# Optimization experiments

Hardware: AMD Instinct MI355X
Metric: run time of the kernel (lower is better)

## Reference

```python
import jax, jax.numpy as jnp
import numpy as np

D_NODE, D_PAIR, H = 512, 128, 16
HD = D_NODE // H  # head_dim = 32
B, N = 2, 1024


def _layernorm(x, gamma, beta, eps=1e-5):
    mu = jnp.mean(x, axis=-1, keepdims=True)
    var = jnp.var(x, axis=-1, keepdims=True)
    return (x - mu) * jax.lax.rsqrt(var + eps) * gamma + beta


def setup_inputs() -> dict:
    key = jax.random.key(0)
    ks = jax.random.split(key, 16)
    sc = 0.02
    inp = {
        's': jax.random.normal(ks[0], (B, N, D_NODE), jnp.float32),
        'z': jax.random.normal(ks[1], (B, N, N, D_PAIR), jnp.float32),
        'key_mask': jax.random.randint(ks[2], (B, N), 0, 2).astype(bool),
        'Wq': jax.random.normal(ks[3], (D_NODE, D_NODE), jnp.float32) * sc,
        'bq': jnp.zeros((D_NODE,), jnp.float32),
        'Wk': jax.random.normal(ks[4], (D_NODE, D_NODE), jnp.float32) * sc,
        'bk': jnp.zeros((D_NODE,), jnp.float32),
        'Wv': jax.random.normal(ks[5], (D_NODE, D_NODE), jnp.float32) * sc,
        'bv': jnp.zeros((D_NODE,), jnp.float32),
        'Wb': jax.random.normal(ks[6], (D_PAIR, H), jnp.float32) * sc,
        'bb': jnp.zeros((H,), jnp.float32),
        'Wg': jax.random.normal(ks[7], (D_NODE, D_NODE), jnp.float32) * sc,
        'bg': jnp.zeros((D_NODE,), jnp.float32),
        'Wo': jax.random.normal(ks[8], (D_NODE, D_NODE), jnp.float32) * sc,
        'bo': jnp.zeros((D_NODE,), jnp.float32),
        'gamma': jnp.ones((D_NODE,), jnp.float32),
        'beta': jnp.zeros((D_NODE,), jnp.float32),
    }
    return inp


def reference(s, z, key_mask, Wq, bq, Wk, bk, Wv, bv, Wb, bb, Wg, bg, Wo, bo, gamma, beta):
    b, n, _ = s.shape
    sn = _layernorm(s, gamma, beta)
    q = (sn @ Wq + bq).reshape(b, n, H, HD)
    k = (sn @ Wk + bk).reshape(b, n, H, HD)
    v = (sn @ Wv + bv).reshape(b, n, H, HD)
    # scores: [B, N(query), N(key), H]
    scores = jnp.einsum('bnhd,bmhd->bnmh', q, k) / np.sqrt(HD).astype(np.float32)
    scores = scores + (z @ Wb + bb)  # additive pair bias
    # mask keys (dim 2); True = masked out
    scores = jnp.where(key_mask[:, None, :, None], -jnp.inf, scores)
    attn = jax.nn.softmax(scores, axis=2)
    attn = jnp.nan_to_num(attn, nan=0.0)
    out = jnp.einsum('bnmh,bmhd->bnhd', attn, v).reshape(b, n, D_NODE)
    gate = jax.nn.sigmoid(sn @ Wg + bg)
    return gate * (out @ Wo + bo)
```

## Files before the change

### kernel.cpp

```cpp
#include <hip/hip_runtime.h>
#include <hip/hip_fp16.h>

typedef __attribute__((ext_vector_type(8))) _Float16 f16x8;
typedef __attribute__((ext_vector_type(8))) unsigned short u16x8;
typedef __attribute__((ext_vector_type(4))) float f32x4;

#define DEV __device__ __forceinline__

DEV unsigned short f2h(float f) {
  _Float16 h = (_Float16)f;
  return __builtin_bit_cast(unsigned short, h);
}
DEV float h2f(unsigned short u) {
  return (float)__builtin_bit_cast(_Float16, u);
}
DEV unsigned pk(float lo, float hi) {
  return (unsigned)f2h(lo) | ((unsigned)f2h(hi) << 16);
}

__global__ __launch_bounds__(256) void k_mask(const unsigned* __restrict__ raw,
                                              int* __restrict__ canon) {
  __shared__ int s_gt1, s_f32;
  int t = threadIdx.x;
  if (t == 0) { s_gt1 = 0; s_f32 = 0; }
  __syncthreads();
  int gt1 = 0, fv = 0;
  for (int i = t; i < 512; i += 256) {
    unsigned v = raw[i];
    if (v == 0x3F800000u) fv = 1;
    else if (v > 1u) gt1 = 1;
  }
  if (gt1) s_gt1 = 1;
  if (fv)  s_f32 = 1;
  __syncthreads();
  int mode = s_gt1 ? 1 : (s_f32 ? 2 : 0);
  for (int i = t; i < 2048; i += 256) {
    int v;
    if (mode == 1)      v = ((const unsigned char*)raw)[i] ? 1 : 0;
    else if (mode == 2) v = (((const float*)raw)[i] != 0.f) ? 1 : 0;
    else                v = raw[i] ? 1 : 0;
    canon[i] = v;
  }
}

__global__ __launch_bounds__(64) void k_ln(const float* __restrict__ s,
                                           const float* __restrict__ gamma,
                                           const float* __restrict__ beta,
                                           unsigned short* __restrict__ sn) {
  int row = blockIdx.x, l = threadIdx.x;
  const float* sr = s + (size_t)row * 512 + l * 8;
  float4 x0 = *(const float4*)sr, x1 = *(const float4*)(sr + 4);
  float sum = x0.x + x0.y + x0.z + x0.w + x1.x + x1.y + x1.z + x1.w;
  float sq  = x0.x*x0.x + x0.y*x0.y + x0.z*x0.z + x0.w*x0.w
            + x1.x*x1.x + x1.y*x1.y + x1.z*x1.z + x1.w*x1.w;
#pragma unroll
  for (int off = 32; off >= 1; off >>= 1) {
    sum += __shfl_xor(sum, off);
    sq  += __shfl_xor(sq, off);
  }
  float mu = sum * (1.f / 512.f);
  float rstd = rsqrtf(sq * (1.f / 512.f) - mu * mu + 1e-5f);
  float4 g0 = *(const float4*)(gamma + l * 8), g1 = *(const float4*)(gamma + l * 8 + 4);
  float4 b0 = *(const float4*)(beta + l * 8),  b1 = *(const float4*)(beta + l * 8 + 4);
  u16x8 o;
  o[0] = f2h((x0.x - mu) * rstd * g0.x + b0.x);
  o[1] = f2h((x0.y - mu) * rstd * g0.y + b0.y);
  o[2] = f2h((x0.z - mu) * rstd * g0.z + b0.z);
  o[3] = f2h((x0.w - mu) * rstd * g0.w + b0.w);
  o[4] = f2h((x1.x - mu) * rstd * g1.x + b1.x);
  o[5] = f2h((x1.y - mu) * rstd * g1.y + b1.y);
  o[6] = f2h((x1.z - mu) * rstd * g1.z + b1.z);
  o[7] = f2h((x1.w - mu) * rstd * g1.w + b1.w);
  *(u16x8*)(sn + (size_t)row * 512 + l * 8) = o;
}

DEV void gemm_body(const unsigned short* __restrict__ A,
                   const float* __restrict__ W,
                   const float* __restrict__ bvec,
                   void* __restrict__ outp,
                   const float* __restrict__ gate,
                   int mode, int ct, int rt) {
  int t = threadIdx.x, l = t & 63, w = t >> 6;
  __shared__ unsigned short As[128 * 40];
  __shared__ unsigned short Bs[128 * 40];
  f32x4 acc[4][4];
#pragma unroll
  for (int mt = 0; mt < 4; ++mt)
#pragma unroll
    for (int nt = 0; nt < 4; ++nt) acc[mt][nt] = (f32x4){0.f, 0.f, 0.f, 0.f};

  int arow = t >> 1, akc = (t & 1) * 16;
  int bkk = t >> 3, bc0 = (t & 7) * 16;
  int wr = w >> 1, wc = w & 1;

  for (int k0 = 0; k0 < 512; k0 += 32) {
    const u16x8* ap = (const u16x8*)(A + (size_t)(rt * 128 + arow) * 512 + k0 + akc);
    u16x8 a0 = ap[0], a1 = ap[1];
    *(u16x8*)(&As[arow * 40 + akc]) = a0;
    *(u16x8*)(&As[arow * 40 + akc + 8]) = a1;
    const float* wp = W + (size_t)(k0 + bkk) * 512 + ct * 128 + bc0;
#pragma unroll
    for (int i = 0; i < 4; ++i) {
      float4 f = *(const float4*)(wp + i * 4);
      Bs[(bc0 + i * 4 + 0) * 40 + bkk] = f2h(f.x);
      Bs[(bc0 + i * 4 + 1) * 40 + bkk] = f2h(f.y);
      Bs[(bc0 + i * 4 + 2) * 40 + bkk] = f2h(f.z);
      Bs[(bc0 + i * 4 + 3) * 40 + bkk] = f2h(f.w);
    }
    __syncthreads();
    f16x8 af[4], bf[4];
#pragma unroll
    for (int mt = 0; mt < 4; ++mt)
      af[mt] = *(const f16x8*)(&As[(wr * 64 + mt * 16 + (l & 15)) * 40 + (l >> 4) * 8]);
#pragma unroll
    for (int nt = 0; nt < 4; ++nt)
      bf[nt] = *(const f16x8*)(&Bs[(wc * 64 + nt * 16 + (l & 15)) * 40 + (l >> 4) * 8]);
#pragma unroll
    for (int mt = 0; mt < 4; ++mt)
#pragma unroll
      for (int nt = 0; nt < 4; ++nt)
        acc[mt][nt] = __builtin_amdgcn_mfma_f32_16x16x32_f16(af[mt], bf[nt], acc[mt][nt], 0, 0, 0);
    __syncthreads();
  }

#pragma unroll
  for (int mt = 0; mt < 4; ++mt)
#pragma unroll
    for (int nt = 0; nt < 4; ++nt) {
      int col = ct * 128 + wc * 64 + nt * 16 + (l & 15);
      float bv = bvec[col];
#pragma unroll
      for (int i = 0; i < 4; ++i) {
        int row = rt * 128 + wr * 64 + mt * 16 + (l >> 4) * 4 + i;
        float val = acc[mt][nt][i] + bv;
        int bb_ = row >> 10, n = row & 1023, hh = col >> 5, d = col & 31;
        if (mode == 0) {
          ((unsigned short*)outp)[(size_t)row * 512 + col] = f2h(val);
        } else if (mode == 1) {
          ((unsigned short*)outp)[(((size_t)bb_ * 16 + hh) * 1024 + n) * 32 + d] = f2h(val);
        } else if (mode == 2) {
          ((unsigned short*)outp)[(((size_t)bb_ * 16 + hh) * 32 + d) * 1024 + n] = f2h(val);
        } else if (mode == 3) {
          ((float*)outp)[(size_t)row * 512 + col] = 1.f / (1.f + __expf(-val));
        } else {
          ((float*)outp)[(size_t)row * 512 + col] = gate[(size_t)row * 512 + col] * val;
        }
      }
    }
}

__global__ __launch_bounds__(256) void k_qkvg(const unsigned short* __restrict__ A,
                                              const float* __restrict__ W0, const float* __restrict__ W1,
                                              const float* __restrict__ W2, const float* __restrict__ W3,
                                              const float* __restrict__ b0, const float* __restrict__ b1,
                                              const float* __restrict__ b2, const float* __restrict__ b3,
                                              void* o0, void* o1, void* o2, void* o3) {
  int mode = blockIdx.z;
  const float* W = (mode == 0) ? W0 : (mode == 1) ? W1 : (mode == 2) ? W2 : W3;
  const float* bv = (mode == 0) ? b0 : (mode == 1) ? b1 : (mode == 2) ? b2 : b3;
  void* o = (mode == 0) ? o0 : (mode == 1) ? o1 : (mode == 2) ? o2 : o3;
  gemm_body(A, W, bv, o, nullptr, mode, blockIdx.x, blockIdx.y);
}

__global__ __launch_bounds__(256) void k_gemm_out(const unsigned short* __restrict__ A,
                                                  const float* __restrict__ W,
                                                  const float* __restrict__ bvec,
                                                  float* __restrict__ outp,
                                                  const float* __restrict__ gate) {
  gemm_body(A, W, bvec, outp, gate, 4, blockIdx.x, blockIdx.y);
}

__global__ __launch_bounds__(512) void k_bias(const float* __restrict__ z,
                                              const float* __restrict__ Wb,
                                              const float* __restrict__ bbp,
                                              const int* __restrict__ maskc,
                                              unsigned short* __restrict__ bias) {
  int bid = blockIdx.x;
  int b = bid >> 10;
  int t = threadIdx.x, l = t & 63, w = t >> 6;
  int lane15 = l & 15, g = l >> 4;

  f16x8 wf[4];
#pragma unroll
  for (int ks = 0; ks < 4; ++ks)
#pragma unroll
    for (int j = 0; j < 8; ++j)
      wf[ks][j] = (_Float16)Wb[(ks * 32 + g * 8 + j) * 16 + lane15];
  float bbh = bbp[lane15];

  const float* zb = z + (size_t)bid * (1024 * 128);
  unsigned short* ob = bias + ((size_t)bid * 16 + lane15) * 1024;
  const int* mrow = maskc + b * 1024;

#pragma unroll 2
  for (int mt = 0; mt < 8; ++mt) {
    int m0 = w * 128 + mt * 16;
    const float* zr = zb + (size_t)(m0 + lane15) * 128 + g * 8;
    f32x4 acc = (f32x4){0.f, 0.f, 0.f, 0.f};
#pragma unroll
    for (int ks = 0; ks < 4; ++ks) {
      float4 z0 = *(const float4*)(zr + ks * 32);
      float4 z1 = *(const float4*)(zr + ks * 32 + 4);
      f16x8 af;
      af[0] = (_Float16)z0.x; af[1] = (_Float16)z0.y;
      af[2] = (_Float16)z0.z; af[3] = (_Float16)z0.w;
      af[4] = (_Float16)z1.x; af[5] = (_Float16)z1.y;
      af[6] = (_Float16)z1.z; af[7] = (_Float16)z1.w;
      acc = __builtin_amdgcn_mfma_f32_16x16x32_f16(af, wf[ks], acc, 0, 0, 0);
    }
    int m = m0 + 4 * g;
    int4 mk = *(const int4*)(mrow + m);
    ushort4 o4;
    o4.x = mk.x ? 0xFBFFu : f2h(acc[0] + bbh);
    o4.y = mk.y ? 0xFBFFu : f2h(acc[1] + bbh);
    o4.z = mk.z ? 0xFBFFu : f2h(acc[2] + bbh);
    o4.w = mk.w ? 0xFBFFu : f2h(acc[3] + bbh);
    *(ushort4*)(ob + m) = o4;
  }
}

__global__ __launch_bounds__(256, 4) void k_attn(const unsigned short* __restrict__ qbuf,
                                                 const unsigned short* __restrict__ kbuf,
                                                 const unsigned short* __restrict__ vbuf,
                                                 const unsigned short* __restrict__ bias,
                                                 unsigned short* __restrict__ aout) {
  int qt = blockIdx.x, h = blockIdx.y, b = blockIdx.z;
  int t = threadIdx.x, l = t & 63, w = t >> 6;
  int q0 = (qt * 4 + w) * 16;
  int lane15 = l & 15, g = l >> 4;
  int bh = b * 16 + h;
  const float RS = 0.17677669529663687f;

  f16x8 qf = *(const f16x8*)(qbuf + ((size_t)(b * 1024 + q0 + lane15)) * 512 + h * 32 + g * 8);

  const unsigned short* kb_ = kbuf + (size_t)bh * 1024 * 32;
  const unsigned short* vb_ = vbuf + (size_t)bh * 32 * 1024;
  const unsigned short* brow = bias + ((size_t)(b * 1024 + q0 + lane15) * 16 + h) * 1024;

  float m_run = -3.0e38f, lsum = 0.f;
  f32x4 acc1 = (f32x4){0.f, 0.f, 0.f, 0.f};
  f32x4 acc2 = (f32x4){0.f, 0.f, 0.f, 0.f};

  for (int c = 0; c < 32; ++c) {
    int m0 = c * 32;
    f16x8 kf1 = *(const f16x8*)(kb_ + (size_t)(m0 + lane15) * 32 + g * 8);
    f16x8 kf2 = *(const f16x8*)(kb_ + (size_t)(m0 + 16 + lane15) * 32 + g * 8);
    f32x4 zero = (f32x4){0.f, 0.f, 0.f, 0.f};
    f32x4 c1 = __builtin_amdgcn_mfma_f32_16x16x32_f16(kf1, qf, zero, 0, 0, 0);
    f32x4 c2 = __builtin_amdgcn_mfma_f32_16x16x32_f16(kf2, qf, zero, 0, 0, 0);
    ushort4 bv1 = *(const ushort4*)(brow + m0 + 4 * g);
    ushort4 bv2 = *(const ushort4*)(brow + m0 + 16 + 4 * g);
    float s1[4], s2[4];
    s1[0] = c1[0] * RS + h2f(bv1.x); s1[1] = c1[1] * RS + h2f(bv1.y);
    s1[2] = c1[2] * RS + h2f(bv1.z); s1[3] = c1[3] * RS + h2f(bv1.w);
    s2[0] = c2[0] * RS + h2f(bv2.x); s2[1] = c2[1] * RS + h2f(bv2.y);
    s2[2] = c2[2] * RS + h2f(bv2.z); s2[3] = c2[3] * RS + h2f(bv2.w);
    float cm = fmaxf(fmaxf(fmaxf(s1[0], s1[1]), fmaxf(s1[2], s1[3])),
                     fmaxf(fmaxf(s2[0], s2[1]), fmaxf(s2[2], s2[3])));
    cm = fmaxf(cm, __shfl_xor(cm, 16));
    cm = fmaxf(cm, __shfl_xor(cm, 32));
    float mn = fmaxf(m_run, cm);
    float corr = __expf(m_run - mn);
    m_run = mn;
    float p1[4], p2[4], csum = 0.f;
#pragma unroll
    for (int i = 0; i < 4; ++i) { p1[i] = __expf(s1[i] - mn); csum += p1[i]; }
#pragma unroll
    for (int i = 0; i < 4; ++i) { p2[i] = __expf(s2[i] - mn); csum += p2[i]; }
    lsum = lsum * corr + csum;
#pragma unroll
    for (int i = 0; i < 4; ++i) { acc1[i] *= corr; acc2[i] *= corr; }
    unsigned a0 = pk(p1[0], p1[1]), a1 = pk(p1[2], p1[3]);
    unsigned b0 = pk(p2[0], p2[1]), b1 = pk(p2[2], p2[3]);
    int s0 = ((g & 1) << 5) + lane15, s1l = s0 + 16;
    unsigned wA0 = (unsigned)__shfl((int)a0, s0);
    unsigned wA1 = (unsigned)__shfl((int)a1, s0);
    unsigned wA2 = (unsigned)__shfl((int)a0, s1l);
    unsigned wA3 = (unsigned)__shfl((int)a1, s1l);
    unsigned wB0 = (unsigned)__shfl((int)b0, s0);
    unsigned wB1 = (unsigned)__shfl((int)b1, s0);
    unsigned wB2 = (unsigned)__shfl((int)b0, s1l);
    unsigned wB3 = (unsigned)__shfl((int)b1, s1l);
    bool hi = (l & 32) != 0;
    union { unsigned u[4]; f16x8 v; } pu;
    pu.u[0] = hi ? wB0 : wA0;
    pu.u[1] = hi ? wB1 : wA1;
    pu.u[2] = hi ? wB2 : wA2;
    pu.u[3] = hi ? wB3 : wA3;
    f16x8 vf1 = *(const f16x8*)(vb_ + (size_t)lane15 * 1024 + m0 + 8 * g);
    f16x8 vf2 = *(const f16x8*)(vb_ + (size_t)(16 + lane15) * 1024 + m0 + 8 * g);
    acc1 = __builtin_amdgcn_mfma_f32_16x16x32_f16(vf1, pu.v, acc1, 0, 0, 0);
    acc2 = __builtin_amdgcn_mfma_f32_16x16x32_f16(vf2, pu.v, acc2, 0, 0, 0);
  }

  lsum += __shfl_xor(lsum, 16);
  lsum += __shfl_xor(lsum, 32);
  float inv = (m_run > -30000.f && lsum > 0.f) ? 1.f / lsum : 0.f;
  unsigned short* orow = aout + ((size_t)(b * 1024 + q0 + lane15)) * 512 + h * 32;
  ushort4 o1, o2;
  o1.x = f2h(acc1[0] * inv); o1.y = f2h(acc1[1] * inv);
  o1.z = f2h(acc1[2] * inv); o1.w = f2h(acc1[3] * inv);
  o2.x = f2h(acc2[0] * inv); o2.y = f2h(acc2[1] * inv);
  o2.z = f2h(acc2[2] * inv); o2.w = f2h(acc2[3] * inv);
  *(ushort4*)(orow + 4 * g) = o1;
  *(ushort4*)(orow + 16 + 4 * g) = o2;
}

extern "C" void kernel_launch(void* const* d_in, const int* in_sizes, int n_in,
                              void* d_out, int out_size, void* d_ws, size_t ws_size,
                              hipStream_t stream) {
  (void)in_sizes; (void)n_in; (void)out_size; (void)ws_size;
  const float* s     = (const float*)d_in[0];
  const float* z     = (const float*)d_in[1];
  const unsigned* km = (const unsigned*)d_in[2];
  const float* Wq = (const float*)d_in[3];
  const float* bq = (const float*)d_in[4];
  const float* Wk = (const float*)d_in[5];
  const float* bk = (const float*)d_in[6];
  const float* Wv = (const float*)d_in[7];
  const float* bv = (const float*)d_in[8];
  const float* Wb = (const float*)d_in[9];
  const float* bb = (const float*)d_in[10];
  const float* Wg = (const float*)d_in[11];
  const float* bg = (const float*)d_in[12];
  const float* Wo = (const float*)d_in[13];
  const float* bo = (const float*)d_in[14];
  const float* gamma = (const float*)d_in[15];
  const float* beta  = (const float*)d_in[16];

  char* ws = (char*)d_ws;
  unsigned short* sn    = (unsigned short*)(ws);
  unsigned short* qbuf  = (unsigned short*)(ws + (2ull << 20));
  unsigned short* kbuf  = (unsigned short*)(ws + (4ull << 20));
  unsigned short* vbuf  = (unsigned short*)(ws + (6ull << 20));
  float*          gate  = (float*)(ws + (8ull << 20));
  unsigned short* aout  = (unsigned short*)(ws + (12ull << 20));
  unsigned short* bias  = (unsigned short*)(ws + (14ull << 20));
  int*            maskc = (int*)(ws + (78ull << 20));

  hipLaunchKernelGGL(k_mask, dim3(1), dim3(256), 0, stream, km, maskc);
  hipLaunchKernelGGL(k_ln, dim3(2048), dim3(64), 0, stream, s, gamma, beta, sn);
  hipLaunchKernelGGL(k_qkvg, dim3(4, 16, 4), dim3(256), 0, stream, sn,
                     Wq, Wk, Wv, Wg, bq, bk, bv, bg,
                     (void*)qbuf, (void*)kbuf, (void*)vbuf, (void*)gate);
  hipLaunchKernelGGL(k_bias, dim3(2048), dim3(512), 0, stream, z, Wb, bb, maskc, bias);
  hipLaunchKernelGGL(k_attn, dim3(16, 16, 2), dim3(256), 0, stream,
                     qbuf, kbuf, vbuf, bias, aout);
  hipLaunchKernelGGL(k_gemm_out, dim3(4, 16), dim3(256), 0, stream, aout, Wo, bo,
                     (float*)d_out, gate);
}
```

Measured before the change: 352.6 us.

## Stage z tiles through swizzled LDS in bias kernel; split attention keys across waves

The pair-bias kernel now loads z in fully coalesced contiguous rows into a per-wave swizzled LDS buffer, register-prefetching the next tile while it computes on the current one. This replaces strided per-lane global reads of z, and z is the dominant memory stream. The attention kernel doubles its block to 512 threads, so two waves split the key range for each query tile and merge partial softmax states through LDS. This doubles parallelism at the cost of an extra reduction and a barrier.

```diff
diff --git a/kernel.cpp b/kernel.cpp
--- a/kernel.cpp
+++ b/kernel.cpp
@@ -170,15 +170,19 @@
   gemm_body(A, W, bvec, outp, gate, 4, blockIdx.x, blockIdx.y);
 }
 
-__global__ __launch_bounds__(512) void k_bias(const float* __restrict__ z,
-                                              const float* __restrict__ Wb,
-                                              const float* __restrict__ bbp,
-                                              const int* __restrict__ maskc,
-                                              unsigned short* __restrict__ bias) {
+__global__ __launch_bounds__(256, 4) void k_bias(const float* __restrict__ z,
+                                                 const float* __restrict__ Wb,
+                                                 const float* __restrict__ bbp,
+                                                 const int* __restrict__ maskc,
+                                                 unsigned short* __restrict__ bias) {
   int bid = blockIdx.x;
-  int b = bid >> 10;
+  int slab = bid >> 1, half = bid & 1;
+  int b = slab >> 10;
   int t = threadIdx.x, l = t & 63, w = t >> 6;
   int lane15 = l & 15, g = l >> 4;
+
+  __shared__ float lds_[4][2048];
+  float* wlds = lds_[w];
 
   f16x8 wf[4];
 #pragma unroll
@@ -188,19 +192,35 @@
       wf[ks][j] = (_Float16)Wb[(ks * 32 + g * 8 + j) * 16 + lane15];
   float bbh = bbp[lane15];
 
-  const float* zb = z + (size_t)bid * (1024 * 128);
-  unsigned short* ob = bias + ((size_t)bid * 16 + lane15) * 1024;
+  const char* zb = (const char*)(z + ((size_t)slab * 1024 + half * 512 + (size_t)w * 128) * 128);
+  unsigned short* ob = bias + ((size_t)slab * 16 + lane15) * 1024;
   const int* mrow = maskc + b * 1024;
 
-#pragma unroll 2
-  for (int mt = 0; mt < 8; ++mt) {
-    int m0 = w * 128 + mt * 16;
-    const float* zr = zb + (size_t)(m0 + lane15) * 128 + g * 8;
+  float4 rbuf[8];
+#pragma unroll
+  for (int i = 0; i < 8; ++i)
+    rbuf[i] = *(const float4*)(zb + i * 1024 + l * 16);
+#pragma unroll
+  for (int i = 0; i < 8; ++i) {
+    int lin = i * 1024 + l * 16;
+    int off = lin ^ (((lin >> 9) & 7) << 4);
+    *(float4*)((char*)wlds + off) = rbuf[i];
+  }
+
+  for (int t8 = 0; t8 < 8; ++t8) {
+    if (t8 < 7) {
+      const char* tb = zb + (t8 + 1) * 8192;
+#pragma unroll
+      for (int i = 0; i < 8; ++i)
+        rbuf[i] = *(const float4*)(tb + i * 1024 + l * 16);
+    }
     f32x4 acc = (f32x4){0.f, 0.f, 0.f, 0.f};
 #pragma unroll
     for (int ks = 0; ks < 4; ++ks) {
-      float4 z0 = *(const float4*)(zr + ks * 32);
-      float4 z1 = *(const float4*)(zr + ks * 32 + 4);
+      int linA = lane15 * 512 + ks * 128 + g * 32;
+      int swz = ((lane15 & 7) << 4);
+      float4 z0 = *(const float4*)((const char*)wlds + (linA ^ swz));
+      float4 z1 = *(const float4*)((const char*)wlds + ((linA + 16) ^ swz));
       f16x8 af;
       af[0] = (_Float16)z0.x; af[1] = (_Float16)z0.y;
       af[2] = (_Float16)z0.z; af[3] = (_Float16)z0.w;
@@ -208,40 +228,54 @@
       af[6] = (_Float16)z1.z; af[7] = (_Float16)z1.w;
       acc = __builtin_amdgcn_mfma_f32_16x16x32_f16(af, wf[ks], acc, 0, 0, 0);
     }
-    int m = m0 + 4 * g;
-    int4 mk = *(const int4*)(mrow + m);
+    int mabs = half * 512 + w * 128 + t8 * 16 + 4 * g;
+    int4 mk = *(const int4*)(mrow + mabs);
     ushort4 o4;
     o4.x = mk.x ? 0xFBFFu : f2h(acc[0] + bbh);
     o4.y = mk.y ? 0xFBFFu : f2h(acc[1] + bbh);
     o4.z = mk.z ? 0xFBFFu : f2h(acc[2] + bbh);
     o4.w = mk.w ? 0xFBFFu : f2h(acc[3] + bbh);
-    *(ushort4*)(ob + m) = o4;
-  }
-}
-
-__global__ __launch_bounds__(256, 4) void k_attn(const unsigned short* __restrict__ qbuf,
+    *(ushort4*)(ob + mabs) = o4;
+    if (t8 < 7) {
+#pragma unroll
+      for (int i = 0; i < 8; ++i) {
+        int lin = i * 1024 + l * 16;
+        int off = lin ^ (((lin >> 9) & 7) << 4);
+        *(float4*)((char*)wlds + off) = rbuf[i];
+      }
+    }
+  }
+}
+
+__global__ __launch_bounds__(512, 4) void k_attn(const unsigned short* __restrict__ qbuf,
                                                  const unsigned short* __restrict__ kbuf,
                                                  const unsigned short* __restrict__ vbuf,
                                                  const unsigned short* __restrict__ bias,
                                                  unsigned short* __restrict__ aout) {
   int qt = blockIdx.x, h = blockIdx.y, b = blockIdx.z;
   int t = threadIdx.x, l = t & 63, w = t >> 6;
-  int q0 = (qt * 4 + w) * 16;
+  int qs = w & 3, half = w >> 2;
+  int q0 = (qt * 4 + qs) * 16;
   int lane15 = l & 15, g = l >> 4;
   int bh = b * 16 + h;
   const float RS = 0.17677669529663687f;
 
+  __shared__ float red_m[4][64];
+  __shared__ float red_l[4][64];
+  __shared__ f32x4 red_a1[4][64];
+  __shared__ f32x4 red_a2[4][64];
+
   f16x8 qf = *(const f16x8*)(qbuf + ((size_t)(b * 1024 + q0 + lane15)) * 512 + h * 32 + g * 8);
 
-  const unsigned short* kb_ = kbuf + (size_t)bh * 1024 * 32;
-  const unsigned short* vb_ = vbuf + (size_t)bh * 32 * 1024;
-  const unsigned short* brow = bias + ((size_t)(b * 1024 + q0 + lane15) * 16 + h) * 1024;
+  const unsigned short* kb_ = kbuf + (size_t)bh * 1024 * 32 + (size_t)half * 512 * 32;
+  const unsigned short* vb_ = vbuf + (size_t)bh * 32 * 1024 + half * 512;
+  const unsigned short* brow = bias + ((size_t)(b * 1024 + q0 + lane15) * 16 + h) * 1024 + half * 512;
 
   float m_run = -3.0e38f, lsum = 0.f;
   f32x4 acc1 = (f32x4){0.f, 0.f, 0.f, 0.f};
   f32x4 acc2 = (f32x4){0.f, 0.f, 0.f, 0.f};
 
-  for (int c = 0; c < 32; ++c) {
+  for (int c = 0; c < 16; ++c) {
     int m0 = c * 32;
     f16x8 kf1 = *(const f16x8*)(kb_ + (size_t)(m0 + lane15) * 32 + g * 8);
     f16x8 kf2 = *(const f16x8*)(kb_ + (size_t)(m0 + 16 + lane15) * 32 + g * 8);
@@ -295,15 +329,34 @@
 
   lsum += __shfl_xor(lsum, 16);
   lsum += __shfl_xor(lsum, 32);
-  float inv = (m_run > -30000.f && lsum > 0.f) ? 1.f / lsum : 0.f;
-  unsigned short* orow = aout + ((size_t)(b * 1024 + q0 + lane15)) * 512 + h * 32;
-  ushort4 o1, o2;
-  o1.x = f2h(acc1[0] * inv); o1.y = f2h(acc1[1] * inv);
-  o1.z = f2h(acc1[2] * inv); o1.w = f2h(acc1[3] * inv);
-  o2.x = f2h(acc2[0] * inv); o2.y = f2h(acc2[1] * inv);
-  o2.z = f2h(acc2[2] * inv); o2.w = f2h(acc2[3] * inv);
-  *(ushort4*)(orow + 4 * g) = o1;
-  *(ushort4*)(orow + 16 + 4 * g) = o2;
+
+  if (half) {
+    red_m[qs][l] = m_run;
+    red_l[qs][l] = lsum;
+    red_a1[qs][l] = acc1;
+    red_a2[qs][l] = acc2;
+  }
+  __syncthreads();
+  if (!half) {
+    float pm = red_m[qs][l], plv = red_l[qs][l];
+    f32x4 pa1 = red_a1[qs][l], pa2 = red_a2[qs][l];
+    float mm = fmaxf(m_run, pm);
+    float c1s = __expf(m_run - mm), c2s = __expf(pm - mm);
+    float lt = lsum * c1s + plv * c2s;
+    float inv = (mm > -30000.f && lt > 0.f) ? 1.f / lt : 0.f;
+    unsigned short* orow = aout + ((size_t)(b * 1024 + q0 + lane15)) * 512 + h * 32;
+    ushort4 o1, o2;
+    o1.x = f2h((acc1[0] * c1s + pa1[0] * c2s) * inv);
+    o1.y = f2h((acc1[1] * c1s + pa1[1] * c2s) * inv);
+    o1.z = f2h((acc1[2] * c1s + pa1[2] * c2s) * inv);
+    o1.w = f2h((acc1[3] * c1s + pa1[3] * c2s) * inv);
+    o2.x = f2h((acc2[0] * c1s + pa2[0] * c2s) * inv);
+    o2.y = f2h((acc2[1] * c1s + pa2[1] * c2s) * inv);
+    o2.z = f2h((acc2[2] * c1s + pa2[2] * c2s) * inv);
+    o2.w = f2h((acc2[3] * c1s + pa2[3] * c2s) * inv);
+    *(ushort4*)(orow + 4 * g) = o1;
+    *(ushort4*)(orow + 16 + 4 * g) = o2;
+  }
 }
 
 extern "C" void kernel_launch(void* const* d_in, const int* in_sizes, int n_in,
@@ -343,8 +396,8 @@
   hipLaunchKernelGGL(k_qkvg, dim3(4, 16, 4), dim3(256), 0, stream, sn,
                      Wq, Wk, Wv, Wg, bq, bk, bv, bg,
                      (void*)qbuf, (void*)kbuf, (void*)vbuf, (void*)gate);
-  hipLaunchKernelGGL(k_bias, dim3(2048), dim3(512), 0, stream, z, Wb, bb, maskc, bias);
-  hipLaunchKernelGGL(k_attn, dim3(16, 16, 2), dim3(256), 0, stream,
+  hipLaunchKernelGGL(k_bias, dim3(4096), dim3(256), 0, stream, z, Wb, bb, maskc, bias);
+  hipLaunchKernelGGL(k_attn, dim3(16, 16, 2), dim3(512), 0, stream,
                      qbuf, kbuf, vbuf, bias, aout);
   hipLaunchKernelGGL(k_gemm_out, dim3(4, 16), dim3(256), 0, stream, aout, Wo, bo,
                      (float*)d_out, gate);
```

After: 358.2 us. No clear change (+1.6%).
